# Kernel optimization log

Hardware: AMD Instinct MI355X
Metric: run time of the kernel (lower is better)

## Reference

```python
import jax, jax.numpy as jnp
import numpy as np

NUM_CLASSES = 80
TOP_K = 200
CONF_T = 0.05
NMS_T = 0.5
CROP = 300.0
A = 49104
B = 8
NEG = -1.0  # dead-score sentinel; real scores are sigmoid outputs in (0,1)


def setup_inputs() -> dict:
    key = jax.random.key(0)
    k1, k2, k3, k4, k5, k6 = jax.random.split(key, 6)
    # structured, plausible anchors in (ymin, xmin, ymax, xmax), pixel coords
    yc = jax.random.uniform(k1, (A,)) * CROP
    xc = jax.random.uniform(k2, (A,)) * CROP
    h = 10.0 + jax.random.uniform(k5, (A,)) * 90.0
    w = 10.0 + jax.random.uniform(k6, (A,)) * 90.0
    anchors = jnp.stack([yc - h / 2, xc - w / 2, yc + h / 2, xc + w / 2], axis=-1)
    confidences = jax.random.normal(k3, (B, A, NUM_CLASSES + 1), dtype=jnp.float32)
    regressions = jax.random.normal(k4, (B, A, 4), dtype=jnp.float32) * 0.1
    return {"confidences": confidences, "regressions": regressions, "anchors": anchors}


def _decode(regressions, anchors):
    yca = (anchors[:, 0] + anchors[:, 2]) / 2
    xca = (anchors[:, 1] + anchors[:, 3]) / 2
    ha = anchors[:, 2] - anchors[:, 0]
    wa = anchors[:, 3] - anchors[:, 1]
    w = jnp.exp(regressions[..., 3]) * wa
    h = jnp.exp(regressions[..., 2]) * ha
    yc = regressions[..., 0] * ha + yca
    xc = regressions[..., 1] * wa + xca
    # clamp exactly as the original: min-clamp on xmin/ymin, max-clamp on xmax/ymax
    xmin = jnp.maximum(xc - w / 2, 0.0) / CROP
    ymin = jnp.maximum(yc - h / 2, 0.0) / CROP
    xmax = jnp.minimum(xc + w / 2, CROP - 1.0) / CROP
    ymax = jnp.minimum(yc + h / 2, CROP - 1.0) / CROP
    return jnp.stack([xmin, ymin, xmax, ymax], axis=-1)  # [B,A,4] (x1,y1,x2,y2)


def _iou_one_to_many(box, boxes):
    x1 = jnp.maximum(box[0], boxes[:, 0])
    y1 = jnp.maximum(box[1], boxes[:, 1])
    x2 = jnp.minimum(box[2], boxes[:, 2])
    y2 = jnp.minimum(box[3], boxes[:, 3])
    inter = jnp.maximum(x2 - x1, 0.0) * jnp.maximum(y2 - y1, 0.0)
    area_b = (box[2] - box[0]) * (box[3] - box[1])
    areas = (boxes[:, 2] - boxes[:, 0]) * (boxes[:, 3] - boxes[:, 1])
    union = area_b + areas - inter
    return jnp.where(union > 0, inter / union, 0.0)


def _nms_image(boxes, probs):
    # boxes: [A,4], probs: [A,C] (sigmoid, background stripped)
    scores = jnp.max(probs, axis=1)
    classes = jnp.argmax(probs, axis=1)
    valid = scores > CONF_T
    # batched_nms trick: offset boxes per class so cross-class IoU is 0
    offset = classes.astype(boxes.dtype) * (jnp.max(boxes) + 1.0)
    boxes_o = boxes + offset[:, None]
    live = jnp.where(valid, scores, NEG)

    def body(live, _):
        idx = jnp.argmax(live)
        keep = live[idx] > 0.0
        iou = _iou_one_to_many(boxes_o[idx], boxes_o)
        live = jnp.where(keep & (iou > NMS_T), NEG, live)
        live = live.at[idx].set(NEG)
        return live, (idx, keep)

    _, (idxs, keeps) = jax.lax.scan(body, live, None, length=TOP_K)
    cls_k = classes[idxs]          # [TOP_K]
    sc_k = scores[idxs]            # [TOP_K]
    bx_k = boxes[idxs]             # [TOP_K,4]
    # per-class slot = rank among kept detections of the same class (keep order is score-descending)
    onehot = (cls_k[:, None] == jnp.arange(NUM_CLASSES)[None, :]) & keeps[:, None]
    slot = jnp.cumsum(onehot, axis=0)[jnp.arange(TOP_K), cls_k] - 1
    rows = jnp.where(keeps, cls_k + 1, NUM_CLASSES + 1)  # OOB row when dropped
    slot = jnp.where(keeps, slot, TOP_K)                 # OOB col when dropped
    vals = jnp.concatenate([sc_k[:, None], bx_k], axis=1)  # [TOP_K,5]
    out = jnp.zeros((NUM_CLASSES + 1, TOP_K, 5), boxes.dtype)
    return out.at[rows, slot].set(vals, mode="drop")


def reference(confidences, regressions, anchors):
    probs = jax.nn.sigmoid(confidences[:, :, 1:])
    boxes = _decode(regressions, anchors)
    return jax.vmap(_nms_image)(boxes, probs)  # [B, C+1, TOP_K, 5]
```

## Files before the change

kernel.cpp:

```cpp
#include <hip/hip_runtime.h>
#include <stdint.h>

#define NCLS 80
#define TOPK 200
#define CONF_T 0.05f
#define CONF_BITS 0x3D4CCCCDu
#define CROPF 300.0f
#define NA 49104
#define NB 8
#define NSEL 256
#define MKEYS 4096
#define APB 64
#define T1 256
#define CHUNK (APB * 81)
#define NGRP (NA / 16)
#define MROW 5
#define OUTFLO ((NCLS + 1) * TOPK * 5)
#define NBLK1 ((NB * NA) / APB)
#define BASE13 125542u
#define NBINS 4512

__device__ __forceinline__ void decode_box(const float4 rg, const float4 an,
                                           float& x1, float& y1, float& x2, float& y2) {
    float yca = (an.x + an.z) * 0.5f;
    float xca = (an.y + an.w) * 0.5f;
    float ha = an.z - an.x;
    float wa = an.w - an.y;
    float w = expf(rg.w) * wa;
    float h = expf(rg.z) * ha;
    float yc = rg.x * ha + yca;
    float xc = rg.y * wa + xca;
    x1 = fmaxf(xc - w * 0.5f, 0.0f) / CROPF;
    y1 = fmaxf(yc - h * 0.5f, 0.0f) / CROPF;
    x2 = fminf(xc + w * 0.5f, CROPF - 1.0f) / CROPF;
    y2 = fminf(yc + h * 0.5f, CROPF - 1.0f) / CROPF;
}

__device__ __forceinline__ float rlf(float v, int l) {
    return __int_as_float(__builtin_amdgcn_readlane(__float_as_int(v), l));
}

__global__ __launch_bounds__(T1) void phase1_kernel(
    const float* __restrict__ conf, const float* __restrict__ reg,
    const float* __restrict__ anch, unsigned long long* __restrict__ key64,
    float4* __restrict__ boxes, float2* __restrict__ gm2,
    float* __restrict__ outz)
{
    __shared__ float lds[CHUNK];
    const int blk = blockIdx.x, t = threadIdx.x;

    {
        const int gid = blk * T1 + t;
        constexpr int TOT4 = NB * OUTFLO / 4;
        if (gid < TOT4)
            reinterpret_cast<float4*>(outz)[gid] = make_float4(0.f, 0.f, 0.f, 0.f);
    }

    const float4* src = reinterpret_cast<const float4*>(conf + (size_t)blk * CHUNK);
    float4* dst = reinterpret_cast<float4*>(lds);
    for (int i = t; i < CHUNK / 4; i += T1) dst[i] = src[i];
    __syncthreads();

    const int la = t >> 2, sub = t & 3;
    const int quad = blk * APB + la;
    const float* crow = lds + la * 81;
    float best = -3.0e38f; int bc = 255;
    #pragma unroll
    for (int k = 0; k < 20; ++k) {
        int c = 1 + sub + 4 * k;
        float v = crow[c];
        if (v > best) { best = v; bc = c; }
    }
    for (int m = 1; m <= 2; m <<= 1) {
        float ov = __shfl_xor(best, m);
        int oc = __shfl_xor(bc, m);
        if (ov > best || (ov == best && oc < bc)) { best = ov; bc = oc; }
    }
    unsigned long long key = 0ull;
    float bmaxl = 0.0f;
    if (sub == 0) {
        int a = quad % NA;
        float s = 1.0f / (1.0f + expf(-best));
        uint32_t ginv = 0x1FFFFu - (uint32_t)a;
        key = ((unsigned long long)__float_as_uint(s) << 32)
            | (unsigned long long)((ginv << 7) | (uint32_t)(bc - 1));
        float4 rg = reinterpret_cast<const float4*>(reg)[quad];
        float4 an = reinterpret_cast<const float4*>(anch)[a];
        float x1, y1, x2, y2; decode_box(rg, an, x1, y1, x2, y2);
        boxes[quad] = make_float4(x1, y1, x2, y2);
        bmaxl = fmaxf(fmaxf(x1, y1), fmaxf(x2, y2));
    }
    {
        const int lane = t & 63, w = t >> 6;
        unsigned long long kk = __shfl(key, (lane & 15) * 4);
        if (lane < 16)
            key64[(size_t)blk * APB + w * 16 + lane] = kk;
    }
    float wbest = best;
    #pragma unroll
    for (int m = 1; m < 64; m <<= 1) {
        wbest = fmaxf(wbest, __shfl_xor(wbest, m));
        bmaxl = fmaxf(bmaxl, __shfl_xor(bmaxl, m));
    }
    if ((t & 63) == 0)
        gm2[blk * 4 + (t >> 6)] = make_float2(1.0f / (1.0f + expf(-wbest)), bmaxl);
}

__device__ __forceinline__ void suffix_scan_1024(uint32_t v, int t,
                                                 uint32_t* wtot, uint32_t* outarr) {
    uint32_t r = v;
    const int lane = t & 63, w = t >> 6;
    #pragma unroll
    for (int m = 1; m < 64; m <<= 1) {
        uint32_t o = __shfl_down(r, m);
        if (lane + m < 64) r += o;
    }
    if (lane == 0) wtot[w] = r;
    __syncthreads();
    if (t < 16) {
        uint32_t v0 = wtot[t], x = v0;
        #pragma unroll
        for (int m = 1; m < 16; m <<= 1) {
            uint32_t o = __shfl_down(x, m);
            if (t + m < 16) x += o;
        }
        wtot[t] = x - v0;
    }
    __syncthreads();
    outarr[t] = r + wtot[w];
    __syncthreads();
}

__global__ __launch_bounds__(1024) void phase2_kernel(
    const unsigned long long* __restrict__ key64, const float4* __restrict__ boxes,
    const float2* __restrict__ gm2, float* __restrict__ out)
{
    __shared__ uint64_t s_keys[MKEYS];
    __shared__ uint64_t s_skeys[MKEYS];
    __shared__ uint64_t s_mask[256 * MROW];
    __shared__ float4   s_boxo[256];
    __shared__ float4   s_braw[256];
    __shared__ float    s_areao[256];
    __shared__ float    s_gm[NGRP + 3];
    __shared__ uint32_t s_glist[2048];
    __shared__ float4   s_keptbox[TOPK];
    __shared__ uint64_t s_clsmask[NCLS][4];
    __shared__ uint32_t s_ccount[NCLS];
    __shared__ uint32_t s_wtot[16];
    __shared__ uint32_t s_shv[12];
    __shared__ float    s_bmaxarr[16];
    __shared__ float    s_offm;
    __shared__ uint8_t  s_clsl[256];
    __shared__ uint64_t s_K[4];

    uint32_t* hist = (uint32_t*)s_keys;
    uint32_t* csum = (uint32_t*)s_skeys;

    const int b = blockIdx.x;
    const int t = threadIdx.x;

    for (int i = t; i < NBINS; i += 1024) hist[i] = 0;
    if (t < 12) s_shv[t] = 0;
    __syncthreads();

    {
        const float2* gmb = gm2 + (size_t)b * NGRP;
        float wm = 0.0f;
        for (int i = t; i < NGRP; i += 1024) {
            float2 v = gmb[i];
            s_gm[i] = v.x;
            wm = fmaxf(wm, v.y);
            if (v.x > CONF_T) {
                int ib = (int)((__float_as_uint(v.x) >> 13) - BASE13);
                ib = max(0, min(NBINS - 1, ib));
                atomicAdd(&hist[ib], 1u);
            }
        }
        #pragma unroll
        for (int m = 1; m < 64; m <<= 1) wm = fmaxf(wm, __shfl_xor(wm, m));
        if ((t & 63) == 0) s_bmaxarr[t >> 6] = wm;
    }
    __syncthreads();

    uint32_t v8 = 0;
    if (t * 8 < NBINS) {
        #pragma unroll
        for (int k = 0; k < 8; ++k) v8 += hist[t * 8 + k];
    }
    suffix_scan_1024(v8, t, s_wtot, csum);
    {
        uint32_t sIn = csum[t];
        uint32_t sNext = (t == 1023) ? 0u : csum[t + 1];
        if (sIn >= NSEL && sNext < NSEL) { s_shv[0] = (uint32_t)t; s_shv[1] = sNext; s_shv[2] = 1; }
    }
    __syncthreads();
    if (t == 0) {
        float mx = s_bmaxarr[0];
        #pragma unroll
        for (int k = 1; k < 16; ++k) mx = fmaxf(mx, s_bmaxarr[k]);
        s_offm = mx + 1.0f;
        if (s_shv[2]) {
            uint32_t chunk = s_shv[0], run2 = s_shv[1]; int cb = -1;
            for (int k = 7; k >= 0; --k) {
                uint32_t v = hist[chunk * 8 + k];
                if (cb < 0 && run2 + v >= NSEL) cb = (int)(chunk * 8 + k);
                run2 += v;
            }
            s_shv[3] = BASE13 + (uint32_t)cb;
        } else s_shv[3] = 0;
    }
    __syncthreads();

    const uint32_t T13 = s_shv[3];
    for (int i = t; i < NGRP; i += 1024) {
        float s = s_gm[i];
        if (s > CONF_T && (__float_as_uint(s) >> 13) >= T13) {
            uint32_t p = atomicAdd(&s_shv[8], 1u);
            if (p < 2048u) s_glist[p] = (uint32_t)i;
        }
    }
    __syncthreads();
    uint32_t ngl = s_shv[8]; if (ngl > 2048u) ngl = 2048u;

    {
        const unsigned long long* kb = key64 + (size_t)b * NA;
        for (int idx = t; idx < (int)(ngl * 16); idx += 1024) {
            uint32_t gi = s_glist[idx >> 4];
            unsigned long long key = kb[gi * 16 + (idx & 15)];
            uint32_t bits = (uint32_t)(key >> 32);
            if (bits > CONF_BITS && (bits >> 13) >= T13) {
                uint32_t p = atomicAdd(&s_shv[4], 1u);
                if (p < MKEYS) s_keys[p] = key;
            }
        }
    }
    __syncthreads();
    uint32_t nGa = s_shv[4]; if (nGa > MKEYS) nGa = MKEYS;
    const int lim = (nGa < 256u) ? (int)nGa : 256;

    {
        const int lane = t & 63;
        const uint32_t nch = (nGa + 63) >> 6;
        for (int s = 0; s < 4; ++s) {
            int kid = t + s * 1024;
            bool act = kid < (int)nGa;
            if (__ballot(act) == 0ull) continue;
            uint64_t my = act ? s_keys[kid] : ~0ull;
            uint32_t r = 0;
            for (uint32_t ch = 0; ch < nch; ++ch) {
                uint32_t src = ch * 64 + (uint32_t)lane;
                uint64_t kc = (src < nGa) ? s_keys[src] : 0ull;
                uint32_t clo = (uint32_t)kc, chi = (uint32_t)(kc >> 32);
                for (int jj = 0; jj < 64; ++jj) {
                    uint32_t olo = (uint32_t)__builtin_amdgcn_readlane((int)clo, jj);
                    uint32_t ohi = (uint32_t)__builtin_amdgcn_readlane((int)chi, jj);
                    uint64_t ok = ((uint64_t)ohi << 32) | olo;
                    r += (ok > my) ? 1u : 0u;
                }
            }
            if (act) s_skeys[r] = my;
        }
    }
    __syncthreads();

    const float offm = s_offm;
    if (t < 256) {
        if (t < lim) {
            uint64_t key = s_skeys[t];
            uint32_t low = (uint32_t)key;
            int c = (int)(low & 0x7Fu);
            uint32_t g = 0x1FFFFu - (low >> 7);
            s_clsl[t] = (uint8_t)c;
            float4 br = boxes[(size_t)b * NA + g];
            s_braw[t] = br;
            float off = (float)c * offm;
            float4 bo = make_float4(br.x + off, br.y + off, br.z + off, br.w + off);
            s_boxo[t] = bo;
            s_areao[t] = (bo.z - bo.x) * (bo.w - bo.y);
        } else {
            s_clsl[t] = 0;
            s_braw[t] = make_float4(0.f, 0.f, 0.f, 0.f);
            s_boxo[t] = make_float4(0.f, 0.f, 0.f, 0.f);
            s_areao[t] = 0.f;
        }
    }
    if (t < NCLS * 4) ((uint64_t*)s_clsmask)[t] = 0ull;
    __syncthreads();

    {
        const int wv = t >> 6, lane = t & 63;
        const int rbase = (wv & 3) * 64, c = wv >> 2;
        const int i = rbase + lane;
        float4 bi = s_boxo[i];
        float aI = s_areao[i];
        float4 vj = s_boxo[c * 64 + lane];
        float vA = s_areao[c * 64 + lane];
        uint64_t m = 0ull;
        for (int jj = 0; jj < 64; ++jj) {
            float bx1 = rlf(vj.x, jj), by1 = rlf(vj.y, jj);
            float bx2 = rlf(vj.z, jj), by2 = rlf(vj.w, jj);
            float aJ  = rlf(vA, jj);
            float ix1 = fmaxf(bi.x, bx1), iy1 = fmaxf(bi.y, by1);
            float ix2 = fminf(bi.z, bx2), iy2 = fminf(bi.w, by2);
            float inter = fmaxf(ix2 - ix1, 0.f) * fmaxf(iy2 - iy1, 0.f);
            float uni = aI + aJ - inter;
            if (uni > 0.f && inter + inter > uni) m |= (1ull << jj);
        }
        s_mask[(size_t)i * MROW + c] = m;
    }
    __syncthreads();

    if (t < 64) {
        const int lane = t;
        uint64_t mr[4][4];
        #pragma unroll
        for (int wr = 0; wr < 4; ++wr)
            #pragma unroll
            for (int wc = 0; wc < 4; ++wc)
                mr[wr][wc] = s_mask[(size_t)(wr * 64 + lane) * MROW + wc];
        const uint64_t below = (lane == 0) ? 0ull : ((~0ull) >> (64 - lane));
        uint64_t K[4];
        #pragma unroll
        for (int w = 0; w < 4; ++w) {
            int lo = w * 64, n = lim - lo;
            K[w] = (n >= 64) ? ~0ull : (n > 0 ? ((~0ull) >> (64 - n)) : 0ull);
        }
        for (int round = 0; round < 257; ++round) {
            uint64_t nK[4];
            #pragma unroll
            for (int wr = 0; wr < 4; ++wr) {
                uint64_t dead = 0ull;
                #pragma unroll
                for (int w = 0; w < 4; ++w) {
                    uint64_t mm = mr[wr][w] & K[w];
                    if (w < wr) dead |= mm;
                    else if (w == wr) dead |= (mm & below);
                }
                bool nb = (dead == 0ull) && (wr * 64 + lane < lim);
                nK[wr] = __ballot(nb);
            }
            bool same = (nK[0] == K[0]) && (nK[1] == K[1]) &&
                        (nK[2] == K[2]) && (nK[3] == K[3]);
            K[0] = nK[0]; K[1] = nK[1]; K[2] = nK[2]; K[3] = nK[3];
            if (same) break;
        }
        if (lane < 4) s_K[lane] = K[lane];
    }
    __syncthreads();

    if (t < 256 && ((s_K[(t >> 6) & 3] >> (t & 63)) & 1ull))
        atomicOr(&s_clsmask[s_clsl[t]][(t >> 6) & 3], 1ull << (t & 63));
    __syncthreads();
    if (t < NCLS) {
        uint32_t n = 0;
        #pragma unroll
        for (int w = 0; w < 4; ++w) n += (uint32_t)__popcll(s_clsmask[t][w]);
        s_ccount[t] = n;
    }
    if (t == 0) {
        uint32_t n = 0;
        #pragma unroll
        for (int w = 0; w < 4; ++w) n += (uint32_t)__popcll(s_K[w]);
        s_shv[7] = n;
    }
    __syncthreads();

    {
        const int jw = (t >> 6) & 3, jb = t & 63;
        bool kept = (t < 256) && ((s_K[jw] >> jb) & 1ull);
        if (kept) {
            const uint64_t below = (jb == 0) ? 0ull : ((~0ull) >> (64 - jb));
            uint32_t ord = (uint32_t)__popcll(s_K[jw] & below);
            for (int w = 0; w < jw; ++w) ord += (uint32_t)__popcll(s_K[w]);
            if (ord < TOPK) {
                int c = (int)s_clsl[t];
                const uint64_t* cm = s_clsmask[c];
                uint32_t slot = (uint32_t)__popcll(cm[jw] & below);
                for (int w = 0; w < jw; ++w) slot += (uint32_t)__popcll(cm[w]);
                float scv = __uint_as_float((uint32_t)(s_skeys[t] >> 32));
                float4 br = s_braw[t];
                float* o = out + (((size_t)b * (NCLS + 1) + (size_t)(c + 1)) * TOPK + slot) * 5;
                o[0] = scv; o[1] = br.x; o[2] = br.y; o[3] = br.z; o[4] = br.w;
                s_keptbox[ord] = s_boxo[t];
            }
        }
    }
    __syncthreads();

    if (t == 0) {
        uint32_t nk = s_shv[7];
        if (nk < TOPK && nGa > (uint32_t)lim) {
            for (uint32_t ci = (uint32_t)lim; ci < nGa && nk < TOPK; ++ci) {
                uint64_t key = s_skeys[ci];
                uint32_t low = (uint32_t)key;
                int c = (int)(low & 0x7Fu);
                uint32_t g = 0x1FFFFu - (low >> 7);
                float4 br = boxes[(size_t)b * NA + g];
                float off = (float)c * offm;
                float4 bo = make_float4(br.x + off, br.y + off, br.z + off, br.w + off);
                float aB2 = (bo.z - bo.x) * (bo.w - bo.y);
                bool sup = false;
                for (uint32_t k2 = 0; k2 < nk && !sup; ++k2) {
                    float4 kb = s_keptbox[k2];
                    float aK = (kb.z - kb.x) * (kb.w - kb.y);
                    float ix1 = fmaxf(bo.x, kb.x), iy1 = fmaxf(bo.y, kb.y);
                    float ix2 = fminf(bo.z, kb.z), iy2 = fminf(bo.w, kb.w);
                    float inter = fmaxf(ix2 - ix1, 0.f) * fmaxf(iy2 - iy1, 0.f);
                    float uni = aB2 + aK - inter;
                    sup = (uni > 0.f && inter + inter > uni);
                }
                if (!sup) {
                    uint32_t slot = s_ccount[c]; s_ccount[c] = slot + 1;
                    float scv = __uint_as_float((uint32_t)(key >> 32));
                    float* o = out + (((size_t)b * (NCLS + 1) + (size_t)(c + 1)) * TOPK + slot) * 5;
                    o[0] = scv; o[1] = br.x; o[2] = br.y; o[3] = br.z; o[4] = br.w;
                    s_keptbox[nk] = bo;
                    ++nk;
                }
            }
        }
    }
}

extern "C" void kernel_launch(void* const* d_in, const int* in_sizes, int n_in,
                              void* d_out, int out_size, void* d_ws, size_t ws_size,
                              hipStream_t stream)
{
    const float* conf = (const float*)d_in[0];
    const float* reg  = (const float*)d_in[1];
    const float* anch = (const float*)d_in[2];
    float* out = (float*)d_out;

    char* ws = (char*)d_ws;
    unsigned long long* key64 = (unsigned long long*)ws;
    float4* boxes = (float4*)(ws + (size_t)NB * NA * 8);
    float2* gm2 = (float2*)(ws + (size_t)NB * NA * 24);

    phase1_kernel<<<NBLK1, T1, 0, stream>>>(conf, reg, anch, key64, boxes, gm2, out);
    phase2_kernel<<<NB, 1024, 0, stream>>>(key64, boxes, gm2, out);
}
```

Baseline: 63.82 us.

## Split per-image phase2 into threshold, parallel gather, and NMS kernels

The single 8-block phase2 kernel becomes three kernels. A threshold kernel computes the histogram cutoff and class offset per image. A wide gather kernel with many blocks compacts qualifying keys and their boxes into a workspace using wave prefix sums and one atomic per block. The NMS kernel then sorts the compacted keys and reads boxes from shared memory rather than doing scattered global box loads. This spreads the gather across the whole GPU instead of 8 blocks, at the cost of two extra launches and workspace round-trips, and it lowers the candidate cap from 4096 to 2048.

```diff
diff --git a/kernel.cpp b/kernel.cpp
--- a/kernel.cpp
+++ b/kernel.cpp
@@ -9,11 +9,12 @@
 #define NA 49104
 #define NB 8
 #define NSEL 256
-#define MKEYS 4096
+#define CKMAX 2048
 #define APB 64
 #define T1 256
 #define CHUNK (APB * 81)
 #define NGRP (NA / 16)
+#define GBLK ((NGRP + 255) / 256)
 #define MROW 5
 #define OUTFLO ((NCLS + 1) * TOPK * 5)
 #define NBLK1 ((NB * NA) / APB)
@@ -131,36 +132,19 @@
     __syncthreads();
 }
 
-__global__ __launch_bounds__(1024) void phase2_kernel(
-    const unsigned long long* __restrict__ key64, const float4* __restrict__ boxes,
-    const float2* __restrict__ gm2, float* __restrict__ out)
+__global__ __launch_bounds__(1024) void phaseT_kernel(
+    const float2* __restrict__ gm2, uint32_t* __restrict__ tg,
+    uint32_t* __restrict__ cnt)
 {
-    __shared__ uint64_t s_keys[MKEYS];
-    __shared__ uint64_t s_skeys[MKEYS];
-    __shared__ uint64_t s_mask[256 * MROW];
-    __shared__ float4   s_boxo[256];
-    __shared__ float4   s_braw[256];
-    __shared__ float    s_areao[256];
-    __shared__ float    s_gm[NGRP + 3];
-    __shared__ uint32_t s_glist[2048];
-    __shared__ float4   s_keptbox[TOPK];
-    __shared__ uint64_t s_clsmask[NCLS][4];
-    __shared__ uint32_t s_ccount[NCLS];
-    __shared__ uint32_t s_wtot[16];
-    __shared__ uint32_t s_shv[12];
-    __shared__ float    s_bmaxarr[16];
-    __shared__ float    s_offm;
-    __shared__ uint8_t  s_clsl[256];
-    __shared__ uint64_t s_K[4];
-
-    uint32_t* hist = (uint32_t*)s_keys;
-    uint32_t* csum = (uint32_t*)s_skeys;
-
-    const int b = blockIdx.x;
-    const int t = threadIdx.x;
-
+    __shared__ uint32_t hist[NBINS];
+    __shared__ uint32_t csum[1024];
+    __shared__ uint32_t wtot[16];
+    __shared__ float    bmaxarr[16];
+    __shared__ uint32_t shv[4];
+
+    const int b = blockIdx.x, t = threadIdx.x;
     for (int i = t; i < NBINS; i += 1024) hist[i] = 0;
-    if (t < 12) s_shv[t] = 0;
+    if (t < 4) shv[t] = 0;
     __syncthreads();
 
     {
@@ -168,7 +152,6 @@
         float wm = 0.0f;
         for (int i = t; i < NGRP; i += 1024) {
             float2 v = gmb[i];
-            s_gm[i] = v.x;
             wm = fmaxf(wm, v.y);
             if (v.x > CONF_T) {
                 int ib = (int)((__float_as_uint(v.x) >> 13) - BASE13);
@@ -178,7 +161,7 @@
         }
         #pragma unroll
         for (int m = 1; m < 64; m <<= 1) wm = fmaxf(wm, __shfl_xor(wm, m));
-        if ((t & 63) == 0) s_bmaxarr[t >> 6] = wm;
+        if ((t & 63) == 0) bmaxarr[t >> 6] = wm;
     }
     __syncthreads();
 
@@ -187,61 +170,128 @@
         #pragma unroll
         for (int k = 0; k < 8; ++k) v8 += hist[t * 8 + k];
     }
-    suffix_scan_1024(v8, t, s_wtot, csum);
+    suffix_scan_1024(v8, t, wtot, csum);
     {
         uint32_t sIn = csum[t];
         uint32_t sNext = (t == 1023) ? 0u : csum[t + 1];
-        if (sIn >= NSEL && sNext < NSEL) { s_shv[0] = (uint32_t)t; s_shv[1] = sNext; s_shv[2] = 1; }
+        if (sIn >= NSEL && sNext < NSEL) { shv[0] = (uint32_t)t; shv[1] = sNext; shv[2] = 1; }
     }
     __syncthreads();
     if (t == 0) {
-        float mx = s_bmaxarr[0];
-        #pragma unroll
-        for (int k = 1; k < 16; ++k) mx = fmaxf(mx, s_bmaxarr[k]);
-        s_offm = mx + 1.0f;
-        if (s_shv[2]) {
-            uint32_t chunk = s_shv[0], run2 = s_shv[1]; int cb = -1;
+        float mx = bmaxarr[0];
+        #pragma unroll
+        for (int k = 1; k < 16; ++k) mx = fmaxf(mx, bmaxarr[k]);
+        uint32_t t13 = 0;
+        if (shv[2]) {
+            uint32_t chunk = shv[0], run2 = shv[1]; int cb = -1;
             for (int k = 7; k >= 0; --k) {
                 uint32_t v = hist[chunk * 8 + k];
                 if (cb < 0 && run2 + v >= NSEL) cb = (int)(chunk * 8 + k);
                 run2 += v;
             }
-            s_shv[3] = BASE13 + (uint32_t)cb;
-        } else s_shv[3] = 0;
-    }
-    __syncthreads();
-
-    const uint32_t T13 = s_shv[3];
-    for (int i = t; i < NGRP; i += 1024) {
-        float s = s_gm[i];
-        if (s > CONF_T && (__float_as_uint(s) >> 13) >= T13) {
-            uint32_t p = atomicAdd(&s_shv[8], 1u);
-            if (p < 2048u) s_glist[p] = (uint32_t)i;
-        }
-    }
-    __syncthreads();
-    uint32_t ngl = s_shv[8]; if (ngl > 2048u) ngl = 2048u;
-
-    {
-        const unsigned long long* kb = key64 + (size_t)b * NA;
-        for (int idx = t; idx < (int)(ngl * 16); idx += 1024) {
-            uint32_t gi = s_glist[idx >> 4];
-            unsigned long long key = kb[gi * 16 + (idx & 15)];
-            uint32_t bits = (uint32_t)(key >> 32);
-            if (bits > CONF_BITS && (bits >> 13) >= T13) {
-                uint32_t p = atomicAdd(&s_shv[4], 1u);
-                if (p < MKEYS) s_keys[p] = key;
-            }
-        }
-    }
-    __syncthreads();
-    uint32_t nGa = s_shv[4]; if (nGa > MKEYS) nGa = MKEYS;
+            t13 = BASE13 + (uint32_t)cb;
+        }
+        tg[2 * b] = t13;
+        tg[2 * b + 1] = __float_as_uint(mx + 1.0f);
+        cnt[b] = 0;
+    }
+}
+
+__global__ __launch_bounds__(256) void phaseG_kernel(
+    const unsigned long long* __restrict__ key64, const float4* __restrict__ boxes,
+    const float2* __restrict__ gm2, const uint32_t* __restrict__ tg,
+    uint32_t* __restrict__ cnt, unsigned long long* __restrict__ ckeys,
+    float4* __restrict__ cboxes)
+{
+    __shared__ uint32_t wsumG[4], woff[4], sbase;
+    const int blk = blockIdx.x, t = threadIdx.x;
+    const int b = blk / GBLK;
+    const int gi = (blk % GBLK) * 256 + t;
+    const uint32_t T13 = tg[2 * b];
+
+    unsigned long long k[16];
+    uint32_t pm = 0; int n = 0;
+    bool qual = false;
+    if (gi < NGRP) {
+        float s = gm2[(size_t)b * NGRP + gi].x;
+        qual = (s > CONF_T) && ((__float_as_uint(s) >> 13) >= T13);
+    }
+    if (qual) {
+        const ulong2* kp = reinterpret_cast<const ulong2*>(key64 + (size_t)b * NA + gi * 16);
+        #pragma unroll
+        for (int j = 0; j < 8; ++j) {
+            ulong2 kk = kp[j];
+            k[2 * j] = kk.x; k[2 * j + 1] = kk.y;
+        }
+        #pragma unroll
+        for (int j = 0; j < 16; ++j) {
+            uint32_t bits = (uint32_t)(k[j] >> 32);
+            if (bits > CONF_BITS && (bits >> 13) >= T13) { pm |= (1u << j); ++n; }
+        }
+    }
+    const int lane = t & 63, w = t >> 6;
+    uint32_t x = (uint32_t)n;
+    #pragma unroll
+    for (int m = 1; m < 64; m <<= 1) {
+        uint32_t o = __shfl_up(x, m);
+        if (lane >= m) x += o;
+    }
+    if (lane == 63) wsumG[w] = x;
+    __syncthreads();
+    if (t == 0) {
+        uint32_t r = 0;
+        #pragma unroll
+        for (int ww = 0; ww < 4; ++ww) { woff[ww] = r; r += wsumG[ww]; }
+        sbase = atomicAdd(&cnt[b], r);
+    }
+    __syncthreads();
+    uint32_t pos = sbase + woff[w] + (x - (uint32_t)n);
+    if (qual && pm) {
+        #pragma unroll
+        for (int j = 0; j < 16; ++j) {
+            if ((pm >> j) & 1u) {
+                if (pos < CKMAX) {
+                    ckeys[(size_t)b * CKMAX + pos] = k[j];
+                    cboxes[(size_t)b * CKMAX + pos] = boxes[(size_t)b * NA + gi * 16 + j];
+                }
+                ++pos;
+            }
+        }
+    }
+}
+
+__global__ __launch_bounds__(1024) void phaseN_kernel(
+    const unsigned long long* __restrict__ ckeys, const float4* __restrict__ cboxes,
+    const uint32_t* __restrict__ tg, const uint32_t* __restrict__ cnt,
+    float* __restrict__ out)
+{
+    __shared__ uint64_t s_keys[CKMAX];
+    __shared__ uint64_t s_skeys[CKMAX];
+    __shared__ float4   s_sbox[CKMAX];
+    __shared__ uint64_t s_mask[256 * MROW];
+    __shared__ float4   s_boxo[256];
+    __shared__ float    s_areao[256];
+    __shared__ float4   s_keptbox[TOPK];
+    __shared__ uint64_t s_clsmask[NCLS][4];
+    __shared__ uint32_t s_ccount[NCLS];
+    __shared__ uint32_t s_shv[4];
+    __shared__ uint8_t  s_clsl[256];
+    __shared__ uint64_t s_K[4];
+
+    const int b = blockIdx.x;
+    const int t = threadIdx.x;
+    uint32_t nGa = cnt[b]; if (nGa > CKMAX) nGa = CKMAX;
     const int lim = (nGa < 256u) ? (int)nGa : 256;
+    const float offm = __uint_as_float(tg[2 * b + 1]);
+
+    for (int i = t; i < (int)nGa; i += 1024)
+        s_keys[i] = ckeys[(size_t)b * CKMAX + i];
+    __syncthreads();
 
     {
         const int lane = t & 63;
         const uint32_t nch = (nGa + 63) >> 6;
-        for (int s = 0; s < 4; ++s) {
+        for (int s = 0; s < CKMAX / 1024; ++s) {
             int kid = t + s * 1024;
             bool act = kid < (int)nGa;
             if (__ballot(act) == 0ull) continue;
@@ -258,28 +308,26 @@
                     r += (ok > my) ? 1u : 0u;
                 }
             }
-            if (act) s_skeys[r] = my;
-        }
-    }
-    __syncthreads();
-
-    const float offm = s_offm;
+            if (act) {
+                s_skeys[r] = my;
+                s_sbox[r] = cboxes[(size_t)b * CKMAX + kid];
+            }
+        }
+    }
+    __syncthreads();
+
     if (t < 256) {
         if (t < lim) {
             uint64_t key = s_skeys[t];
-            uint32_t low = (uint32_t)key;
-            int c = (int)(low & 0x7Fu);
-            uint32_t g = 0x1FFFFu - (low >> 7);
+            int c = (int)((uint32_t)key & 0x7Fu);
             s_clsl[t] = (uint8_t)c;
-            float4 br = boxes[(size_t)b * NA + g];
-            s_braw[t] = br;
+            float4 br = s_sbox[t];
             float off = (float)c * offm;
             float4 bo = make_float4(br.x + off, br.y + off, br.z + off, br.w + off);
             s_boxo[t] = bo;
             s_areao[t] = (bo.z - bo.x) * (bo.w - bo.y);
         } else {
             s_clsl[t] = 0;
-            s_braw[t] = make_float4(0.f, 0.f, 0.f, 0.f);
             s_boxo[t] = make_float4(0.f, 0.f, 0.f, 0.f);
             s_areao[t] = 0.f;
         }
@@ -361,7 +409,7 @@
         uint32_t n = 0;
         #pragma unroll
         for (int w = 0; w < 4; ++w) n += (uint32_t)__popcll(s_K[w]);
-        s_shv[7] = n;
+        s_shv[0] = n;
     }
     __syncthreads();
 
@@ -378,7 +426,7 @@
                 uint32_t slot = (uint32_t)__popcll(cm[jw] & below);
                 for (int w = 0; w < jw; ++w) slot += (uint32_t)__popcll(cm[w]);
                 float scv = __uint_as_float((uint32_t)(s_skeys[t] >> 32));
-                float4 br = s_braw[t];
+                float4 br = s_sbox[t];
                 float* o = out + (((size_t)b * (NCLS + 1) + (size_t)(c + 1)) * TOPK + slot) * 5;
                 o[0] = scv; o[1] = br.x; o[2] = br.y; o[3] = br.z; o[4] = br.w;
                 s_keptbox[ord] = s_boxo[t];
@@ -388,14 +436,12 @@
     __syncthreads();
 
     if (t == 0) {
-        uint32_t nk = s_shv[7];
+        uint32_t nk = s_shv[0];
         if (nk < TOPK && nGa > (uint32_t)lim) {
             for (uint32_t ci = (uint32_t)lim; ci < nGa && nk < TOPK; ++ci) {
                 uint64_t key = s_skeys[ci];
-                uint32_t low = (uint32_t)key;
-                int c = (int)(low & 0x7Fu);
-                uint32_t g = 0x1FFFFu - (low >> 7);
-                float4 br = boxes[(size_t)b * NA + g];
+                int c = (int)((uint32_t)key & 0x7Fu);
+                float4 br = s_sbox[ci];
                 float off = (float)c * offm;
                 float4 bo = make_float4(br.x + off, br.y + off, br.z + off, br.w + off);
                 float aB2 = (bo.z - bo.x) * (bo.w - bo.y);
@@ -435,7 +481,14 @@
     unsigned long long* key64 = (unsigned long long*)ws;
     float4* boxes = (float4*)(ws + (size_t)NB * NA * 8);
     float2* gm2 = (float2*)(ws + (size_t)NB * NA * 24);
+    char* p = ws + (size_t)NB * NA * 24 + (size_t)NB * NGRP * 8;
+    uint32_t* tg = (uint32_t*)p;
+    uint32_t* cnt = (uint32_t*)(p + 64);
+    unsigned long long* ckeys = (unsigned long long*)(p + 256);
+    float4* cboxes = (float4*)(p + 256 + (size_t)NB * CKMAX * 8);
 
     phase1_kernel<<<NBLK1, T1, 0, stream>>>(conf, reg, anch, key64, boxes, gm2, out);
-    phase2_kernel<<<NB, 1024, 0, stream>>>(key64, boxes, gm2, out);
-}
+    phaseT_kernel<<<NB, 1024, 0, stream>>>(gm2, tg, cnt);
+    phaseG_kernel<<<NB * GBLK, 256, 0, stream>>>(key64, boxes, gm2, tg, cnt, ckeys, cboxes);
+    phaseN_kernel<<<NB, 1024, 0, stream>>>(ckeys, cboxes, tg, cnt, out);
+}
```

Result: slower. 69.45 us (+8.8%).

## Streamline threshold search and candidate gather to cut block barriers in NMS phase

Applied to the files above, without the earlier changes.

Replaces the 1024-thread suffix scan over histogram bins with a single-wavefront scan over 71-bin runs, computed alongside the box-max reduction in a second wave. The two-pass group list and key gather is merged into one pass where each qualifying group thread loads its 16 keys directly. Per-class counts and the kept total are now computed lazily by thread 0, only when the fallback path runs, and the clsmask clear is moved to the start. These changes remove several __syncthreads and a shared buffer. The cost is more serial work in one wave and less parallelism in the key gather.

```diff
diff --git a/kernel.cpp b/kernel.cpp
--- a/kernel.cpp
+++ b/kernel.cpp
@@ -19,6 +19,7 @@
 #define NBLK1 ((NB * NA) / APB)
 #define BASE13 125542u
 #define NBINS 4512
+#define RUNL 71
 
 __device__ __forceinline__ void decode_box(const float4 rg, const float4 an,
                                            float& x1, float& y1, float& x2, float& y2) {
@@ -106,61 +107,34 @@
         gm2[blk * 4 + (t >> 6)] = make_float2(1.0f / (1.0f + expf(-wbest)), bmaxl);
 }
 
-__device__ __forceinline__ void suffix_scan_1024(uint32_t v, int t,
-                                                 uint32_t* wtot, uint32_t* outarr) {
-    uint32_t r = v;
-    const int lane = t & 63, w = t >> 6;
-    #pragma unroll
-    for (int m = 1; m < 64; m <<= 1) {
-        uint32_t o = __shfl_down(r, m);
-        if (lane + m < 64) r += o;
-    }
-    if (lane == 0) wtot[w] = r;
-    __syncthreads();
-    if (t < 16) {
-        uint32_t v0 = wtot[t], x = v0;
-        #pragma unroll
-        for (int m = 1; m < 16; m <<= 1) {
-            uint32_t o = __shfl_down(x, m);
-            if (t + m < 16) x += o;
-        }
-        wtot[t] = x - v0;
-    }
-    __syncthreads();
-    outarr[t] = r + wtot[w];
-    __syncthreads();
-}
-
 __global__ __launch_bounds__(1024) void phase2_kernel(
     const unsigned long long* __restrict__ key64, const float4* __restrict__ boxes,
     const float2* __restrict__ gm2, float* __restrict__ out)
 {
     __shared__ uint64_t s_keys[MKEYS];
     __shared__ uint64_t s_skeys[MKEYS];
+    __shared__ float    s_gm[NGRP + 3];
     __shared__ uint64_t s_mask[256 * MROW];
     __shared__ float4   s_boxo[256];
     __shared__ float4   s_braw[256];
     __shared__ float    s_areao[256];
-    __shared__ float    s_gm[NGRP + 3];
-    __shared__ uint32_t s_glist[2048];
     __shared__ float4   s_keptbox[TOPK];
     __shared__ uint64_t s_clsmask[NCLS][4];
     __shared__ uint32_t s_ccount[NCLS];
-    __shared__ uint32_t s_wtot[16];
-    __shared__ uint32_t s_shv[12];
+    __shared__ uint32_t s_shv[8];
     __shared__ float    s_bmaxarr[16];
     __shared__ float    s_offm;
     __shared__ uint8_t  s_clsl[256];
     __shared__ uint64_t s_K[4];
 
     uint32_t* hist = (uint32_t*)s_keys;
-    uint32_t* csum = (uint32_t*)s_skeys;
 
     const int b = blockIdx.x;
     const int t = threadIdx.x;
 
     for (int i = t; i < NBINS; i += 1024) hist[i] = 0;
-    if (t < 12) s_shv[t] = 0;
+    if (t < NCLS * 4) ((uint64_t*)s_clsmask)[t] = 0ull;
+    if (t < 8) s_shv[t] = 0;
     __syncthreads();
 
     {
@@ -182,32 +156,44 @@
     }
     __syncthreads();
 
-    uint32_t v8 = 0;
-    if (t * 8 < NBINS) {
-        #pragma unroll
-        for (int k = 0; k < 8; ++k) v8 += hist[t * 8 + k];
-    }
-    suffix_scan_1024(v8, t, s_wtot, csum);
-    {
-        uint32_t sIn = csum[t];
-        uint32_t sNext = (t == 1023) ? 0u : csum[t + 1];
-        if (sIn >= NSEL && sNext < NSEL) { s_shv[0] = (uint32_t)t; s_shv[1] = sNext; s_shv[2] = 1; }
-    }
-    __syncthreads();
-    if (t == 0) {
-        float mx = s_bmaxarr[0];
-        #pragma unroll
-        for (int k = 1; k < 16; ++k) mx = fmaxf(mx, s_bmaxarr[k]);
-        s_offm = mx + 1.0f;
-        if (s_shv[2]) {
-            uint32_t chunk = s_shv[0], run2 = s_shv[1]; int cb = -1;
-            for (int k = 7; k >= 0; --k) {
-                uint32_t v = hist[chunk * 8 + k];
-                if (cb < 0 && run2 + v >= NSEL) cb = (int)(chunk * 8 + k);
-                run2 += v;
-            }
-            s_shv[3] = BASE13 + (uint32_t)cb;
-        } else s_shv[3] = 0;
+    if (t < 64) {
+        const int lane = t;
+        uint32_t run = 0;
+        const int base = lane * RUNL;
+        #pragma unroll
+        for (int k = 0; k < RUNL; ++k) {
+            int ib = base + k;
+            run += (ib < NBINS) ? hist[ib] : 0u;
+        }
+        uint32_t S = run;
+        #pragma unroll
+        for (int m = 1; m < 64; m <<= 1) {
+            uint32_t o = __shfl_down(S, m);
+            if (lane + m < 64) S += o;
+        }
+        uint64_t bal = __ballot(S >= NSEL);
+        int L = bal ? (63 - __builtin_clzll(bal)) : -1;
+        uint32_t SnextL = (L >= 0 && L < 63)
+            ? (uint32_t)__builtin_amdgcn_readlane((int)S, L + 1) : 0u;
+        if (lane == 0) {
+            uint32_t t13 = 0;
+            if (L >= 0) {
+                uint32_t running = SnextL;
+                for (int k = RUNL - 1; k >= 0; --k) {
+                    int ib = L * RUNL + k;
+                    if (ib >= NBINS) continue;
+                    running += hist[ib];
+                    if (running >= NSEL) { t13 = BASE13 + (uint32_t)ib; break; }
+                }
+            }
+            s_shv[3] = t13;
+        }
+    } else if (t < 128) {
+        const int lane2 = t - 64;
+        float m = (lane2 < 16) ? s_bmaxarr[lane2] : 0.0f;
+        #pragma unroll
+        for (int s = 1; s < 64; s <<= 1) m = fmaxf(m, __shfl_xor(m, s));
+        if (lane2 == 0) s_offm = m + 1.0f;
     }
     __syncthreads();
 
@@ -215,22 +201,15 @@
     for (int i = t; i < NGRP; i += 1024) {
         float s = s_gm[i];
         if (s > CONF_T && (__float_as_uint(s) >> 13) >= T13) {
-            uint32_t p = atomicAdd(&s_shv[8], 1u);
-            if (p < 2048u) s_glist[p] = (uint32_t)i;
-        }
-    }
-    __syncthreads();
-    uint32_t ngl = s_shv[8]; if (ngl > 2048u) ngl = 2048u;
-
-    {
-        const unsigned long long* kb = key64 + (size_t)b * NA;
-        for (int idx = t; idx < (int)(ngl * 16); idx += 1024) {
-            uint32_t gi = s_glist[idx >> 4];
-            unsigned long long key = kb[gi * 16 + (idx & 15)];
-            uint32_t bits = (uint32_t)(key >> 32);
-            if (bits > CONF_BITS && (bits >> 13) >= T13) {
-                uint32_t p = atomicAdd(&s_shv[4], 1u);
-                if (p < MKEYS) s_keys[p] = key;
+            const unsigned long long* kp = key64 + (size_t)b * NA + (size_t)i * 16;
+            #pragma unroll
+            for (int j = 0; j < 16; ++j) {
+                unsigned long long key = kp[j];
+                uint32_t bits = (uint32_t)(key >> 32);
+                if (bits > CONF_BITS && (bits >> 13) >= T13) {
+                    uint32_t p = atomicAdd(&s_shv[4], 1u);
+                    if (p < MKEYS) s_keys[p] = key;
+                }
             }
         }
     }
@@ -241,7 +220,7 @@
     {
         const int lane = t & 63;
         const uint32_t nch = (nGa + 63) >> 6;
-        for (int s = 0; s < 4; ++s) {
+        for (int s = 0; s < MKEYS / 1024; ++s) {
             int kid = t + s * 1024;
             bool act = kid < (int)nGa;
             if (__ballot(act) == 0ull) continue;
@@ -284,7 +263,6 @@
             s_areao[t] = 0.f;
         }
     }
-    if (t < NCLS * 4) ((uint64_t*)s_clsmask)[t] = 0ull;
     __syncthreads();
 
     {
@@ -351,19 +329,6 @@
     if (t < 256 && ((s_K[(t >> 6) & 3] >> (t & 63)) & 1ull))
         atomicOr(&s_clsmask[s_clsl[t]][(t >> 6) & 3], 1ull << (t & 63));
     __syncthreads();
-    if (t < NCLS) {
-        uint32_t n = 0;
-        #pragma unroll
-        for (int w = 0; w < 4; ++w) n += (uint32_t)__popcll(s_clsmask[t][w]);
-        s_ccount[t] = n;
-    }
-    if (t == 0) {
-        uint32_t n = 0;
-        #pragma unroll
-        for (int w = 0; w < 4; ++w) n += (uint32_t)__popcll(s_K[w]);
-        s_shv[7] = n;
-    }
-    __syncthreads();
 
     {
         const int jw = (t >> 6) & 3, jb = t & 63;
@@ -388,8 +353,16 @@
     __syncthreads();
 
     if (t == 0) {
-        uint32_t nk = s_shv[7];
+        uint32_t nk = 0;
+        #pragma unroll
+        for (int w = 0; w < 4; ++w) nk += (uint32_t)__popcll(s_K[w]);
         if (nk < TOPK && nGa > (uint32_t)lim) {
+            for (int c = 0; c < NCLS; ++c) {
+                uint32_t n = 0;
+                #pragma unroll
+                for (int w = 0; w < 4; ++w) n += (uint32_t)__popcll(s_clsmask[c][w]);
+                s_ccount[c] = n;
+            }
             for (uint32_t ci = (uint32_t)lim; ci < nGa && nk < TOPK; ++ci) {
                 uint64_t key = s_skeys[ci];
                 uint32_t low = (uint32_t)key;
```

Measured after the change: 71.34 us. 11.8% more time.

## Fuse both phases into one cooperative kernel with grid sync

Applied to the files above, without the earlier changes.

Replaces the two-kernel launch with a single cooperative kernel. Its 256 persistent blocks first loop over confidence chunks to do the argmax/decode stage, then synchronize the grid, and the first 8 blocks run the per-image NMS. Shared memory is unioned between stages. Per-class counts are now computed only in the serial fallback path, which removes one barrier. This targets the inter-kernel launch gap but lowers occupancy and memory-level parallelism in the bandwidth-bound first stage.

```diff
diff --git a/kernel.cpp b/kernel.cpp
--- a/kernel.cpp
+++ b/kernel.cpp
@@ -1,4 +1,5 @@
 #include <hip/hip_runtime.h>
+#include <hip/hip_cooperative_groups.h>
 #include <stdint.h>
 
 #define NCLS 80
@@ -10,15 +11,16 @@
 #define NB 8
 #define NSEL 256
 #define MKEYS 4096
-#define APB 64
-#define T1 256
-#define CHUNK (APB * 81)
 #define NGRP (NA / 16)
 #define MROW 5
 #define OUTFLO ((NCLS + 1) * TOPK * 5)
-#define NBLK1 ((NB * NA) / APB)
+#define NCHUNK ((NB * NA) / 64)
 #define BASE13 125542u
 #define NBINS 4512
+#define NBLKS 256
+#define C81 5184
+
+namespace cg = cooperative_groups;
 
 __device__ __forceinline__ void decode_box(const float4 rg, const float4 an,
                                            float& x1, float& y1, float& x2, float& y2) {
@@ -40,72 +42,6 @@
     return __int_as_float(__builtin_amdgcn_readlane(__float_as_int(v), l));
 }
 
-__global__ __launch_bounds__(T1) void phase1_kernel(
-    const float* __restrict__ conf, const float* __restrict__ reg,
-    const float* __restrict__ anch, unsigned long long* __restrict__ key64,
-    float4* __restrict__ boxes, float2* __restrict__ gm2,
-    float* __restrict__ outz)
-{
-    __shared__ float lds[CHUNK];
-    const int blk = blockIdx.x, t = threadIdx.x;
-
-    {
-        const int gid = blk * T1 + t;
-        constexpr int TOT4 = NB * OUTFLO / 4;
-        if (gid < TOT4)
-            reinterpret_cast<float4*>(outz)[gid] = make_float4(0.f, 0.f, 0.f, 0.f);
-    }
-
-    const float4* src = reinterpret_cast<const float4*>(conf + (size_t)blk * CHUNK);
-    float4* dst = reinterpret_cast<float4*>(lds);
-    for (int i = t; i < CHUNK / 4; i += T1) dst[i] = src[i];
-    __syncthreads();
-
-    const int la = t >> 2, sub = t & 3;
-    const int quad = blk * APB + la;
-    const float* crow = lds + la * 81;
-    float best = -3.0e38f; int bc = 255;
-    #pragma unroll
-    for (int k = 0; k < 20; ++k) {
-        int c = 1 + sub + 4 * k;
-        float v = crow[c];
-        if (v > best) { best = v; bc = c; }
-    }
-    for (int m = 1; m <= 2; m <<= 1) {
-        float ov = __shfl_xor(best, m);
-        int oc = __shfl_xor(bc, m);
-        if (ov > best || (ov == best && oc < bc)) { best = ov; bc = oc; }
-    }
-    unsigned long long key = 0ull;
-    float bmaxl = 0.0f;
-    if (sub == 0) {
-        int a = quad % NA;
-        float s = 1.0f / (1.0f + expf(-best));
-        uint32_t ginv = 0x1FFFFu - (uint32_t)a;
-        key = ((unsigned long long)__float_as_uint(s) << 32)
-            | (unsigned long long)((ginv << 7) | (uint32_t)(bc - 1));
-        float4 rg = reinterpret_cast<const float4*>(reg)[quad];
-        float4 an = reinterpret_cast<const float4*>(anch)[a];
-        float x1, y1, x2, y2; decode_box(rg, an, x1, y1, x2, y2);
-        boxes[quad] = make_float4(x1, y1, x2, y2);
-        bmaxl = fmaxf(fmaxf(x1, y1), fmaxf(x2, y2));
-    }
-    {
-        const int lane = t & 63, w = t >> 6;
-        unsigned long long kk = __shfl(key, (lane & 15) * 4);
-        if (lane < 16)
-            key64[(size_t)blk * APB + w * 16 + lane] = kk;
-    }
-    float wbest = best;
-    #pragma unroll
-    for (int m = 1; m < 64; m <<= 1) {
-        wbest = fmaxf(wbest, __shfl_xor(wbest, m));
-        bmaxl = fmaxf(bmaxl, __shfl_xor(bmaxl, m));
-    }
-    if ((t & 63) == 0)
-        gm2[blk * 4 + (t >> 6)] = make_float2(1.0f / (1.0f + expf(-wbest)), bmaxl);
-}
-
 __device__ __forceinline__ void suffix_scan_1024(uint32_t v, int t,
                                                  uint32_t* wtot, uint32_t* outarr) {
     uint32_t r = v;
@@ -131,33 +67,136 @@
     __syncthreads();
 }
 
-__global__ __launch_bounds__(1024) void phase2_kernel(
-    const unsigned long long* __restrict__ key64, const float4* __restrict__ boxes,
-    const float2* __restrict__ gm2, float* __restrict__ out)
+struct PhaseB {
+    uint64_t s_keys[MKEYS];
+    uint64_t s_skeys[MKEYS];
+    float    s_gm[NGRP + 3];
+    uint64_t s_mask[256 * MROW];
+    float4   s_boxo[256];
+    float4   s_braw[256];
+    float    s_areao[256];
+    float4   s_keptbox[TOPK];
+    uint64_t s_clsmask[NCLS][4];
+    uint32_t s_ccount[NCLS];
+    uint32_t s_glist[2048];
+    uint32_t s_wtot[16];
+    uint32_t s_shv[12];
+    float    s_bmaxarr[16];
+    float    s_offm;
+    uint8_t  s_clsl[256];
+    uint64_t s_K[4];
+};
+
+union SharedU {
+    float  stageA[4 * C81];
+    PhaseB b;
+};
+
+__global__ __launch_bounds__(1024, 1) void fused_kernel(
+    const float* __restrict__ conf, const float* __restrict__ reg,
+    const float* __restrict__ anch, unsigned long long* __restrict__ key64,
+    float4* __restrict__ boxes, float2* __restrict__ gm2,
+    float* __restrict__ out)
 {
-    __shared__ uint64_t s_keys[MKEYS];
-    __shared__ uint64_t s_skeys[MKEYS];
-    __shared__ uint64_t s_mask[256 * MROW];
-    __shared__ float4   s_boxo[256];
-    __shared__ float4   s_braw[256];
-    __shared__ float    s_areao[256];
-    __shared__ float    s_gm[NGRP + 3];
-    __shared__ uint32_t s_glist[2048];
-    __shared__ float4   s_keptbox[TOPK];
-    __shared__ uint64_t s_clsmask[NCLS][4];
-    __shared__ uint32_t s_ccount[NCLS];
-    __shared__ uint32_t s_wtot[16];
-    __shared__ uint32_t s_shv[12];
-    __shared__ float    s_bmaxarr[16];
-    __shared__ float    s_offm;
-    __shared__ uint8_t  s_clsl[256];
-    __shared__ uint64_t s_K[4];
-
+    __shared__ SharedU sh;
+    cg::grid_group grid = cg::this_grid();
+    const int blk = blockIdx.x, t = threadIdx.x;
+
+    {
+        const int gid = blk * 1024 + t;
+        constexpr int TOT4 = NB * OUTFLO / 4;
+        if (gid < TOT4)
+            reinterpret_cast<float4*>(out)[gid] = make_float4(0.f, 0.f, 0.f, 0.f);
+    }
+
+    for (int k = 0; ; ++k) {
+        const int q0 = blk * 4 + k * 1024;
+        if (q0 >= NCHUNK) break;
+        const int nch = min(4, NCHUNK - q0);
+        {
+            const float4* src = reinterpret_cast<const float4*>(conf + (size_t)q0 * C81);
+            float4* dst = reinterpret_cast<float4*>(sh.stageA);
+            const int n4 = nch * (C81 / 4);
+            for (int i = t; i < n4; i += 1024) dst[i] = src[i];
+        }
+        __syncthreads();
+
+        const int j = t >> 8;
+        const bool act = (j < nch);
+        const int tid = t & 255;
+        const int la = tid >> 2, sub = tid & 3;
+        const int chunk = q0 + j;
+        const int quad = chunk * 64 + la;
+        const float* crow = sh.stageA + j * C81 + la * 81;
+        float best = -3.0e38f; int bc = 255;
+        if (act) {
+            #pragma unroll
+            for (int k2 = 0; k2 < 20; ++k2) {
+                int c = 1 + sub + 4 * k2;
+                float v = crow[c];
+                if (v > best) { best = v; bc = c; }
+            }
+        }
+        for (int m = 1; m <= 2; m <<= 1) {
+            float ov = __shfl_xor(best, m);
+            int oc = __shfl_xor(bc, m);
+            if (ov > best || (ov == best && oc < bc)) { best = ov; bc = oc; }
+        }
+        unsigned long long key = 0ull;
+        float bmaxl = 0.0f;
+        if (act && sub == 0) {
+            int a = quad % NA;
+            float s = 1.0f / (1.0f + expf(-best));
+            uint32_t ginv = 0x1FFFFu - (uint32_t)a;
+            key = ((unsigned long long)__float_as_uint(s) << 32)
+                | (unsigned long long)((ginv << 7) | (uint32_t)(bc - 1));
+            float4 rg = reinterpret_cast<const float4*>(reg)[quad];
+            float4 an = reinterpret_cast<const float4*>(anch)[a];
+            float x1, y1, x2, y2; decode_box(rg, an, x1, y1, x2, y2);
+            boxes[quad] = make_float4(x1, y1, x2, y2);
+            bmaxl = fmaxf(fmaxf(x1, y1), fmaxf(x2, y2));
+        }
+        {
+            const int lane = t & 63, wl = (t >> 6) & 3;
+            unsigned long long kk = __shfl(key, (lane & 15) * 4);
+            if (act && lane < 16)
+                key64[(size_t)chunk * 64 + wl * 16 + lane] = kk;
+        }
+        float wbest = best;
+        #pragma unroll
+        for (int m = 1; m < 64; m <<= 1) {
+            wbest = fmaxf(wbest, __shfl_xor(wbest, m));
+            bmaxl = fmaxf(bmaxl, __shfl_xor(bmaxl, m));
+        }
+        if (act && (t & 63) == 0)
+            gm2[chunk * 4 + ((t >> 6) & 3)] =
+                make_float2(1.0f / (1.0f + expf(-wbest)), bmaxl);
+        __syncthreads();
+    }
+
+    grid.sync();
+
+    if (blk >= NB) return;
+    const int b = blk;
+
+    uint64_t (&s_keys)[MKEYS] = sh.b.s_keys;
+    uint64_t (&s_skeys)[MKEYS] = sh.b.s_skeys;
+    float (&s_gm)[NGRP + 3] = sh.b.s_gm;
+    uint64_t (&s_mask)[256 * MROW] = sh.b.s_mask;
+    float4 (&s_boxo)[256] = sh.b.s_boxo;
+    float4 (&s_braw)[256] = sh.b.s_braw;
+    float (&s_areao)[256] = sh.b.s_areao;
+    float4 (&s_keptbox)[TOPK] = sh.b.s_keptbox;
+    uint64_t (&s_clsmask)[NCLS][4] = sh.b.s_clsmask;
+    uint32_t (&s_ccount)[NCLS] = sh.b.s_ccount;
+    uint32_t (&s_glist)[2048] = sh.b.s_glist;
+    uint32_t (&s_wtot)[16] = sh.b.s_wtot;
+    uint32_t (&s_shv)[12] = sh.b.s_shv;
+    float (&s_bmaxarr)[16] = sh.b.s_bmaxarr;
+    uint8_t (&s_clsl)[256] = sh.b.s_clsl;
+    uint64_t (&s_K)[4] = sh.b.s_K;
     uint32_t* hist = (uint32_t*)s_keys;
     uint32_t* csum = (uint32_t*)s_skeys;
-
-    const int b = blockIdx.x;
-    const int t = threadIdx.x;
 
     for (int i = t; i < NBINS; i += 1024) hist[i] = 0;
     if (t < 12) s_shv[t] = 0;
@@ -198,7 +237,7 @@
         float mx = s_bmaxarr[0];
         #pragma unroll
         for (int k = 1; k < 16; ++k) mx = fmaxf(mx, s_bmaxarr[k]);
-        s_offm = mx + 1.0f;
+        sh.b.s_offm = mx + 1.0f;
         if (s_shv[2]) {
             uint32_t chunk = s_shv[0], run2 = s_shv[1]; int cb = -1;
             for (int k = 7; k >= 0; --k) {
@@ -240,14 +279,14 @@
 
     {
         const int lane = t & 63;
-        const uint32_t nch = (nGa + 63) >> 6;
-        for (int s = 0; s < 4; ++s) {
+        const uint32_t nch2 = (nGa + 63) >> 6;
+        for (int s = 0; s < MKEYS / 1024; ++s) {
             int kid = t + s * 1024;
-            bool act = kid < (int)nGa;
-            if (__ballot(act) == 0ull) continue;
-            uint64_t my = act ? s_keys[kid] : ~0ull;
+            bool act2 = kid < (int)nGa;
+            if (__ballot(act2) == 0ull) continue;
+            uint64_t my = act2 ? s_keys[kid] : ~0ull;
             uint32_t r = 0;
-            for (uint32_t ch = 0; ch < nch; ++ch) {
+            for (uint32_t ch = 0; ch < nch2; ++ch) {
                 uint32_t src = ch * 64 + (uint32_t)lane;
                 uint64_t kc = (src < nGa) ? s_keys[src] : 0ull;
                 uint32_t clo = (uint32_t)kc, chi = (uint32_t)(kc >> 32);
@@ -258,12 +297,12 @@
                     r += (ok > my) ? 1u : 0u;
                 }
             }
-            if (act) s_skeys[r] = my;
-        }
-    }
-    __syncthreads();
-
-    const float offm = s_offm;
+            if (act2) s_skeys[r] = my;
+        }
+    }
+    __syncthreads();
+
+    const float offm = sh.b.s_offm;
     if (t < 256) {
         if (t < lim) {
             uint64_t key = s_skeys[t];
@@ -351,19 +390,6 @@
     if (t < 256 && ((s_K[(t >> 6) & 3] >> (t & 63)) & 1ull))
         atomicOr(&s_clsmask[s_clsl[t]][(t >> 6) & 3], 1ull << (t & 63));
     __syncthreads();
-    if (t < NCLS) {
-        uint32_t n = 0;
-        #pragma unroll
-        for (int w = 0; w < 4; ++w) n += (uint32_t)__popcll(s_clsmask[t][w]);
-        s_ccount[t] = n;
-    }
-    if (t == 0) {
-        uint32_t n = 0;
-        #pragma unroll
-        for (int w = 0; w < 4; ++w) n += (uint32_t)__popcll(s_K[w]);
-        s_shv[7] = n;
-    }
-    __syncthreads();
 
     {
         const int jw = (t >> 6) & 3, jb = t & 63;
@@ -388,8 +414,16 @@
     __syncthreads();
 
     if (t == 0) {
-        uint32_t nk = s_shv[7];
+        uint32_t nk = 0;
+        #pragma unroll
+        for (int w = 0; w < 4; ++w) nk += (uint32_t)__popcll(s_K[w]);
         if (nk < TOPK && nGa > (uint32_t)lim) {
+            for (int c = 0; c < NCLS; ++c) {
+                uint32_t n = 0;
+                #pragma unroll
+                for (int w = 0; w < 4; ++w) n += (uint32_t)__popcll(s_clsmask[c][w]);
+                s_ccount[c] = n;
+            }
             for (uint32_t ci = (uint32_t)lim; ci < nGa && nk < TOPK; ++ci) {
                 uint64_t key = s_skeys[ci];
                 uint32_t low = (uint32_t)key;
@@ -436,6 +470,8 @@
     float4* boxes = (float4*)(ws + (size_t)NB * NA * 8);
     float2* gm2 = (float2*)(ws + (size_t)NB * NA * 24);
 
-    phase1_kernel<<<NBLK1, T1, 0, stream>>>(conf, reg, anch, key64, boxes, gm2, out);
-    phase2_kernel<<<NB, 1024, 0, stream>>>(key64, boxes, gm2, out);
+    void* args[] = { (void*)&conf, (void*)&reg, (void*)&anch,
+                     (void*)&key64, (void*)&boxes, (void*)&gm2, (void*)&out };
+    hipLaunchCooperativeKernel((const void*)fused_kernel, dim3(NBLKS), dim3(1024),
+                               args, 0, stream);
 }
```

Result: slower. 113.4 us (+77.8%).
